# Kernel tuning notes

Measured on AMD Instinct MI355X. Metric: run time of the kernel, lower is better.

## Reference

```python
import jax, jax.numpy as jnp
import numpy as np

EPS = 1e-6
N_HEADS = 16


def _stable_softmax(x):
    # max subtracted with stop_gradient (torch .detach()), clamp to [-50, 50], eps in denom
    x_max = jax.lax.stop_gradient(jnp.max(x, axis=-1, keepdims=True))
    exp_x = jnp.exp(jnp.clip(x - x_max, -50.0, 50.0))
    return exp_x / (jnp.sum(exp_x, axis=-1, keepdims=True) + EPS)


def setup_inputs() -> dict:
    key = jax.random.key(0)
    k1, k2, k3 = jax.random.split(key, 3)
    B, S, D = 2, 2048, 1024
    x = jax.random.normal(k1, (B, S, D), dtype=jnp.float32)
    Wqkv = jax.random.normal(k2, (3 * D, D), dtype=jnp.float32) * 0.02
    Wout = jax.random.normal(k3, (D, D), dtype=jnp.float32) * (0.02 / np.sqrt(2))
    return {"x": x, "Wqkv": Wqkv, "Wout": Wout}


def reference(x, Wqkv, Wout):
    B, S, D = x.shape
    H = N_HEADS
    Dh = D // H
    scale = 1.0 / np.sqrt(Dh)
    # qkv projection (torch Linear: x @ W.T), split into q,k,v -> (B,H,S,Dh)
    qkv = (x @ Wqkv.T).reshape(B, S, 3, H, Dh)
    qkv = jnp.transpose(qkv, (2, 0, 3, 1, 4))
    q, k, v = qkv[0], qkv[1], qkv[2]
    # chunked attention is mathematically identical to full attention here
    scores = jnp.einsum('bhqd,bhkd->bhqk', q, k) * scale
    attn = _stable_softmax(scores)
    out = jnp.einsum('bhqk,bhkd->bhqd', attn, v)  # (B,H,S,Dh)
    out = jnp.transpose(out, (0, 2, 1, 3)).reshape(B, S, D)
    return out @ Wout.T
```

## Files before the change

kernel.cpp:

```cpp
#include <hip/hip_runtime.h>
#include <hip/hip_bf16.h>
#include <stdint.h>

#define S_LEN   2048
#define D_MODEL 1024
#define NH      16
#define DH      64
#define BATCH   2
#define TOKENS  (BATCH * S_LEN)

typedef __bf16 bf16;
typedef __bf16 bf16x8 __attribute__((ext_vector_type(8)));
typedef __bf16 b16x4  __attribute__((ext_vector_type(4)));
typedef float  f32x4  __attribute__((ext_vector_type(4)));
typedef float  f32x16 __attribute__((ext_vector_type(16)));
typedef unsigned int uint32;

__device__ __forceinline__ void async_lds16(const void* g, void* l) {
  __builtin_amdgcn_global_load_lds((__attribute__((address_space(1))) void*)g,
                                   (__attribute__((address_space(3))) void*)l,
                                   16, 0, 0);
}

__global__ __launch_bounds__(256) void convert_kernel(
    const float* __restrict__ src, bf16* __restrict__ dst, int n8) {
  const int i = blockIdx.x * 256 + threadIdx.x;
  if (i >= n8) return;
  const f32x4 a = *(const f32x4*)(src + (size_t)i * 8);
  const f32x4 b = *(const f32x4*)(src + (size_t)i * 8 + 4);
  bf16x8 o;
#pragma unroll
  for (int j = 0; j < 4; j++) { o[j] = (bf16)a[j]; o[j + 4] = (bf16)b[j]; }
  *(bf16x8*)(dst + (size_t)i * 8) = o;
}

#define BM 128
#define BN 128
#define BK 32

#define GEMM_CORE(APTR, BPTR, KDIM)                                              \
  __shared__ __align__(16) bf16 As[BM * BK];                                     \
  __shared__ __align__(16) bf16 Bs[BN * BK];                                     \
  const int tid  = threadIdx.x;                                                  \
  const int wave = tid >> 6, lane = tid & 63;                                    \
  const int quad = lane >> 4, l16 = lane & 15;                                   \
  const int m0 = blockIdx.y * BM;                                                \
  const int n0 = blockIdx.x * BN;                                                \
  const int wm = (wave >> 1) * 64, wn = (wave & 1) * 64;                         \
  f32x4 acc[4][4] = {};                                                          \
  const int c0 = tid, c1 = tid + 256;                                            \
  for (int k0 = 0; k0 < (KDIM); k0 += BK) {                                      \
    async_lds16((APTR) + (size_t)(m0 + (c0 >> 2)) * (KDIM) + k0 + (c0 & 3) * 8,  \
                As + c0 * 8);                                                    \
    async_lds16((APTR) + (size_t)(m0 + (c1 >> 2)) * (KDIM) + k0 + (c1 & 3) * 8,  \
                As + c1 * 8);                                                    \
    async_lds16((BPTR) + (size_t)(n0 + (c0 >> 2)) * (KDIM) + k0 + (c0 & 3) * 8,  \
                Bs + c0 * 8);                                                    \
    async_lds16((BPTR) + (size_t)(n0 + (c1 >> 2)) * (KDIM) + k0 + (c1 & 3) * 8,  \
                Bs + c1 * 8);                                                    \
    __syncthreads();                                                             \
    bf16x8 af[4], bfr[4];                                                        \
    _Pragma("unroll") for (int i = 0; i < 4; i++)                                \
        af[i] = *(const bf16x8*)(As + (wm + i * 16 + l16) * BK + quad * 8);      \
    _Pragma("unroll") for (int j = 0; j < 4; j++)                                \
        bfr[j] = *(const bf16x8*)(Bs + (wn + j * 16 + l16) * BK + quad * 8);     \
    _Pragma("unroll") for (int i = 0; i < 4; i++)                                \
      _Pragma("unroll") for (int j = 0; j < 4; j++)                              \
        acc[i][j] = __builtin_amdgcn_mfma_f32_16x16x32_bf16(af[i], bfr[j],       \
                                                            acc[i][j], 0, 0, 0); \
    __syncthreads();                                                             \
  }

__global__ __launch_bounds__(256) void gemm_qkv_kernel(
    const bf16* __restrict__ X, const bf16* __restrict__ W,
    bf16* __restrict__ Qo, bf16* __restrict__ Ko, bf16* __restrict__ VTo) {
  GEMM_CORE(X, W, D_MODEL)
  const int t = n0 >> 10;
#pragma unroll
  for (int i = 0; i < 4; i++) {
    const int rowb = m0 + wm + i * 16 + quad * 4;
    const int b = rowb >> 11, s0 = rowb & 2047;
#pragma unroll
    for (int j = 0; j < 4; j++) {
      const int col = n0 + wn + j * 16 + l16;
      const int h = (col >> 6) & 15, d = col & 63;
      if (t == 2) {
        b16x4 v4;
#pragma unroll
        for (int r = 0; r < 4; r++) v4[r] = (bf16)acc[i][j][r];
        *(b16x4*)(VTo + ((size_t)(b * NH + h) * DH + d) * S_LEN + s0) = v4;
      } else {
#pragma unroll
        for (int r = 0; r < 4; r++) {
          const float v = acc[i][j][r];
          if (t == 0)
            Qo[((size_t)(b * NH + h) * S_LEN + s0 + r) * DH + d] = (bf16)(v * 0.125f);
          else
            Ko[((size_t)(b * NH + h) * S_LEN + s0 + r) * DH + d] = (bf16)v;
        }
      }
    }
  }
}

__global__ __launch_bounds__(256) void gemm_out_kernel(
    const bf16* __restrict__ A, const bf16* __restrict__ W,
    float* __restrict__ Out) {
  GEMM_CORE(A, W, D_MODEL)
#pragma unroll
  for (int i = 0; i < 4; i++) {
    const int rowb = m0 + wm + i * 16 + quad * 4;
#pragma unroll
    for (int j = 0; j < 4; j++) {
      const int col = n0 + wn + j * 16 + l16;
#pragma unroll
      for (int r = 0; r < 4; r++)
        Out[(size_t)(rowb + r) * D_MODEL + col] = acc[i][j][r];
    }
  }
}

__global__ __launch_bounds__(512, 4) void attn_kernel(
    const bf16* __restrict__ Q, const bf16* __restrict__ K,
    const bf16* __restrict__ VT, bf16* __restrict__ AO) {
  __shared__ __align__(16) bf16 smem[2][2][2 * 64 * 64];

  const int tid  = threadIdx.x;
  const int lane = tid & 63;
  const int wave = tid >> 6;
  const int g    = wave >> 2;
  const int qw   = wave & 3;
  const int l31  = lane & 31;
  const int hi   = lane >> 5;
  const int sw   = l31 & 7;

  const int bid = (blockIdx.x & 7) * 64 + (blockIdx.x >> 3);
  const int qb  = bid & 15;
  const int bh  = bid >> 4;

  const bf16* qp = Q  + ((size_t)bh * S_LEN + qb * 128 + qw * 32 + l31) * DH;
  const bf16* kp = K  + (size_t)bh * S_LEN * DH;
  const bf16* vp = VT + (size_t)bh * DH * S_LEN;

  bf16x8 qf[4];
#pragma unroll
  for (int dk = 0; dk < 4; dk++)
    qf[dk] = *(const bf16x8*)(qp + dk * 16 + hi * 8);

  const int gtid = tid & 255;
  const int cid0 = gtid, cid1 = gtid + 256;
  const int r0 = cid0 >> 3, c0 = (cid0 & 7) ^ (r0 & 7);
  const int r1 = cid1 >> 3, c1 = (cid1 & 7) ^ (r1 & 7);
  const bf16* ka0 = kp + (size_t)(g * 64 + r0) * DH + c0 * 8;
  const bf16* ka1 = kp + (size_t)(g * 64 + r1) * DH + c1 * 8;
  const bf16* va0 = vp + (size_t)r0 * S_LEN + g * 64 + c0 * 8;
  const bf16* va1 = vp + (size_t)r1 * S_LEN + g * 64 + c1 * 8;
  const int ld0 = cid0 * 8, ld1 = cid1 * 8;

  f32x16 oT[2] = {};
  float lsum = 0.f;

  bf16* sg = &smem[g][0][0];

#define STAGE(B)                                                                 \
  {                                                                              \
    bf16* s = sg + (B) * (2 * 64 * 64);                                          \
    async_lds16(ka0, s + ld0);                                                   \
    async_lds16(ka1, s + ld1);                                                   \
    async_lds16(va0, s + 4096 + ld0);                                            \
    async_lds16(va1, s + 4096 + ld1);                                            \
    ka0 += 8192; ka1 += 8192; va0 += 128; va1 += 128;                            \
  }

  STAGE(0)

  for (int t = 0; t < 16; t++) {
    const int cur = t & 1;
    if (t < 15) {
      STAGE(cur ^ 1)
      asm volatile("s_waitcnt vmcnt(4)" ::: "memory");
    } else {
      asm volatile("s_waitcnt vmcnt(0)" ::: "memory");
    }
    __builtin_amdgcn_s_barrier();
    __builtin_amdgcn_s_setprio(1);

    const bf16* sb = sg + cur * (2 * 64 * 64);

    f32x16 st[2] = {};
#pragma unroll
    for (int kt = 0; kt < 2; kt++)
#pragma unroll
      for (int dk = 0; dk < 4; dk++) {
        const bf16x8 kf = *(const bf16x8*)(sb + (kt * 32 + l31) * 64 +
                                           (((dk * 2 + hi) ^ sw) * 8));
        st[kt] = __builtin_amdgcn_mfma_f32_32x32x16_bf16(kf, qf[dk], st[kt], 0, 0, 0);
      }

#pragma unroll
    for (int kt = 0; kt < 2; kt++)
#pragma unroll
      for (int half = 0; half < 2; half++) {
        float e[8];
#pragma unroll
        for (int r = 0; r < 8; r++) e[r] = __expf(st[kt][half * 8 + r]);
        lsum += ((e[0] + e[1]) + (e[2] + e[3])) + ((e[4] + e[5]) + (e[6] + e[7]));
        uint32 a0, a1, b0, b1;
        asm("v_cvt_pk_bf16_f32 %0, %1, %2" : "=v"(a0) : "v"(e[0]), "v"(e[1]));
        asm("v_cvt_pk_bf16_f32 %0, %1, %2" : "=v"(a1) : "v"(e[2]), "v"(e[3]));
        asm("v_cvt_pk_bf16_f32 %0, %1, %2" : "=v"(b0) : "v"(e[4]), "v"(e[5]));
        asm("v_cvt_pk_bf16_f32 %0, %1, %2" : "=v"(b1) : "v"(e[6]), "v"(e[7]));
        asm("v_permlane32_swap_b32 %0, %1" : "+v"(a0), "+v"(b0));
        asm("v_permlane32_swap_b32 %0, %1" : "+v"(a1), "+v"(b1));
        union { uint32 u[4]; bf16x8 v; } pf;
        pf.u[0] = a0; pf.u[1] = a1; pf.u[2] = b0; pf.u[3] = b1;
        const int ks = kt * 2 + half;
#pragma unroll
        for (int dt = 0; dt < 2; dt++) {
          const bf16x8 vf = *(const bf16x8*)(sb + 4096 + (dt * 32 + l31) * 64 +
                                             (((ks * 2 + hi) ^ sw) * 8));
          oT[dt] = __builtin_amdgcn_mfma_f32_32x32x16_bf16(vf, pf.v, oT[dt], 0, 0, 0);
        }
      }

    __builtin_amdgcn_s_setprio(0);
    asm volatile("s_waitcnt lgkmcnt(0)" ::: "memory");
    __builtin_amdgcn_s_barrier();
  }
#undef STAGE

  lsum += __shfl_xor(lsum, 32);

  float* mO = (float*)&smem[0][0][0];
  float* mL = mO + 4 * 64 * 32;
  const int mrow = qw * 64 + lane;
  if (g == 1) {
#pragma unroll
    for (int j = 0; j < 8; j++) {
      const int dt = j >> 2, rb = (j & 3) * 4;
      f32x4 c = { oT[dt][rb], oT[dt][rb + 1], oT[dt][rb + 2], oT[dt][rb + 3] };
      *(f32x4*)((char*)mO + mrow * 128 + ((j ^ (lane & 7)) * 16)) = c;
    }
    mL[mrow] = lsum;
  }
  __syncthreads();
  if (g == 0) {
#pragma unroll
    for (int j = 0; j < 8; j++) {
      const int dt = j >> 2, rb = (j & 3) * 4;
      const f32x4 c = *(const f32x4*)((char*)mO + mrow * 128 + ((j ^ (lane & 7)) * 16));
#pragma unroll
      for (int rr = 0; rr < 4; rr++) oT[dt][rb + rr] += c[rr];
    }
    lsum += mL[mrow];
    const float inv = 1.0f / (lsum + 1e-6f);
    const int b = bh >> 4, h = bh & 15;
    const int srow = qb * 128 + qw * 32 + l31;
    const size_t base = (size_t)(b * S_LEN + srow) * D_MODEL + h * DH;
#pragma unroll
    for (int dt = 0; dt < 2; dt++)
#pragma unroll
      for (int rg = 0; rg < 4; rg++) {
        b16x4 o4;
#pragma unroll
        for (int rr = 0; rr < 4; rr++) o4[rr] = (bf16)(oT[dt][rg * 4 + rr] * inv);
        *(b16x4*)(AO + base + dt * 32 + rg * 8 + hi * 4) = o4;
      }
  }
}

extern "C" void kernel_launch(void* const* d_in, const int* in_sizes, int n_in,
                              void* d_out, int out_size, void* d_ws, size_t ws_size,
                              hipStream_t stream) {
  const float* x    = (const float*)d_in[0];
  const float* wqkv = (const float*)d_in[1];
  const float* wout = (const float*)d_in[2];
  float* out = (float*)d_out;

  bf16* Q  = (bf16*)d_ws;
  bf16* K  = Q  + (size_t)TOKENS * D_MODEL;
  bf16* VT = K  + (size_t)TOKENS * D_MODEL;
  bf16* xb = VT + (size_t)TOKENS * D_MODEL;
  bf16* AO = xb;
  bf16* wqkvb = (bf16*)d_out;
  bf16* woutb = Q;

  convert_kernel<<<dim3(TOKENS * D_MODEL / (256 * 8)), dim3(256), 0, stream>>>(
      x, xb, TOKENS * D_MODEL / 8);
  convert_kernel<<<dim3(3 * D_MODEL * D_MODEL / (256 * 8)), dim3(256), 0, stream>>>(
      wqkv, wqkvb, 3 * D_MODEL * D_MODEL / 8);

  gemm_qkv_kernel<<<dim3(3 * D_MODEL / BN, TOKENS / BM), dim3(256), 0, stream>>>(
      xb, wqkvb, Q, K, VT);

  attn_kernel<<<dim3(BATCH * NH * (S_LEN / 128)), dim3(512), 0, stream>>>(Q, K, VT, AO);

  convert_kernel<<<dim3(D_MODEL * D_MODEL / (256 * 8)), dim3(256), 0, stream>>>(
      wout, woutb, D_MODEL * D_MODEL / 8);

  gemm_out_kernel<<<dim3(D_MODEL / BN, TOKENS / BM), dim3(256), 0, stream>>>(
      AO, woutb, out);
}
```

Baseline: 187.9 us.

## Process two 32-row query tiles per wave in attention to reuse K/V fragments

Each attention wave now handles 64 query rows (two 32-row MFMA tiles) instead of 32, so each block covers 256 queries and the grid is halved. Every K and V fragment read from LDS feeds two MFMAs, which halves LDS traffic and global K/V staging per query. The cost is double the accumulator registers, so launch bounds drop to 2 blocks per CU, and the cross-group merge now takes two serialized rounds through shared memory. Fewer blocks (256) may underfill the GPU's compute units.

```diff
diff --git a/kernel.cpp b/kernel.cpp
--- a/kernel.cpp
+++ b/kernel.cpp
@@ -120,7 +120,7 @@
   }
 }
 
-__global__ __launch_bounds__(512, 4) void attn_kernel(
+__global__ __launch_bounds__(512, 2) void attn_kernel(
     const bf16* __restrict__ Q, const bf16* __restrict__ K,
     const bf16* __restrict__ VT, bf16* __restrict__ AO) {
   __shared__ __align__(16) bf16 smem[2][2][2 * 64 * 64];
@@ -134,18 +134,20 @@
   const int hi   = lane >> 5;
   const int sw   = l31 & 7;
 
-  const int bid = (blockIdx.x & 7) * 64 + (blockIdx.x >> 3);
-  const int qb  = bid & 15;
-  const int bh  = bid >> 4;
-
-  const bf16* qp = Q  + ((size_t)bh * S_LEN + qb * 128 + qw * 32 + l31) * DH;
+  const int bid = (blockIdx.x & 7) * 32 + (blockIdx.x >> 3);
+  const int qb  = bid & 7;
+  const int bh  = bid >> 3;
+
+  const bf16* qp = Q  + ((size_t)bh * S_LEN + qb * 256 + qw * 64 + l31) * DH;
   const bf16* kp = K  + (size_t)bh * S_LEN * DH;
   const bf16* vp = VT + (size_t)bh * DH * S_LEN;
 
-  bf16x8 qf[4];
-#pragma unroll
-  for (int dk = 0; dk < 4; dk++)
-    qf[dk] = *(const bf16x8*)(qp + dk * 16 + hi * 8);
+  bf16x8 qf0[4], qf1[4];
+#pragma unroll
+  for (int dk = 0; dk < 4; dk++) {
+    qf0[dk] = *(const bf16x8*)(qp + dk * 16 + hi * 8);
+    qf1[dk] = *(const bf16x8*)(qp + 32 * DH + dk * 16 + hi * 8);
+  }
 
   const int gtid = tid & 255;
   const int cid0 = gtid, cid1 = gtid + 256;
@@ -157,8 +159,8 @@
   const bf16* va1 = vp + (size_t)r1 * S_LEN + g * 64 + c1 * 8;
   const int ld0 = cid0 * 8, ld1 = cid1 * 8;
 
-  f32x16 oT[2] = {};
-  float lsum = 0.f;
+  f32x16 oT0[2] = {}, oT1[2] = {};
+  float lsum0 = 0.f, lsum1 = 0.f;
 
   bf16* sg = &smem[g][0][0];
 
@@ -187,39 +189,51 @@
 
     const bf16* sb = sg + cur * (2 * 64 * 64);
 
-    f32x16 st[2] = {};
+    f32x16 st0[2] = {}, st1[2] = {};
 #pragma unroll
     for (int kt = 0; kt < 2; kt++)
 #pragma unroll
       for (int dk = 0; dk < 4; dk++) {
         const bf16x8 kf = *(const bf16x8*)(sb + (kt * 32 + l31) * 64 +
                                            (((dk * 2 + hi) ^ sw) * 8));
-        st[kt] = __builtin_amdgcn_mfma_f32_32x32x16_bf16(kf, qf[dk], st[kt], 0, 0, 0);
+        st0[kt] = __builtin_amdgcn_mfma_f32_32x32x16_bf16(kf, qf0[dk], st0[kt], 0, 0, 0);
+        st1[kt] = __builtin_amdgcn_mfma_f32_32x32x16_bf16(kf, qf1[dk], st1[kt], 0, 0, 0);
       }
 
 #pragma unroll
     for (int kt = 0; kt < 2; kt++)
 #pragma unroll
-      for (int half = 0; half < 2; half++) {
-        float e[8];
-#pragma unroll
-        for (int r = 0; r < 8; r++) e[r] = __expf(st[kt][half * 8 + r]);
-        lsum += ((e[0] + e[1]) + (e[2] + e[3])) + ((e[4] + e[5]) + (e[6] + e[7]));
-        uint32 a0, a1, b0, b1;
-        asm("v_cvt_pk_bf16_f32 %0, %1, %2" : "=v"(a0) : "v"(e[0]), "v"(e[1]));
-        asm("v_cvt_pk_bf16_f32 %0, %1, %2" : "=v"(a1) : "v"(e[2]), "v"(e[3]));
-        asm("v_cvt_pk_bf16_f32 %0, %1, %2" : "=v"(b0) : "v"(e[4]), "v"(e[5]));
-        asm("v_cvt_pk_bf16_f32 %0, %1, %2" : "=v"(b1) : "v"(e[6]), "v"(e[7]));
-        asm("v_permlane32_swap_b32 %0, %1" : "+v"(a0), "+v"(b0));
-        asm("v_permlane32_swap_b32 %0, %1" : "+v"(a1), "+v"(b1));
-        union { uint32 u[4]; bf16x8 v; } pf;
-        pf.u[0] = a0; pf.u[1] = a1; pf.u[2] = b0; pf.u[3] = b1;
-        const int ks = kt * 2 + half;
+      for (int hk = 0; hk < 2; hk++) {
+        const int ks = kt * 2 + hk;
+        float e0[8], e1[8];
+#pragma unroll
+        for (int r = 0; r < 8; r++) e0[r] = __expf(st0[kt][hk * 8 + r]);
+#pragma unroll
+        for (int r = 0; r < 8; r++) e1[r] = __expf(st1[kt][hk * 8 + r]);
+        lsum0 += ((e0[0] + e0[1]) + (e0[2] + e0[3])) + ((e0[4] + e0[5]) + (e0[6] + e0[7]));
+        lsum1 += ((e1[0] + e1[1]) + (e1[2] + e1[3])) + ((e1[4] + e1[5]) + (e1[6] + e1[7]));
+        uint32 p00, p01, p02, p03, p10, p11, p12, p13;
+        asm("v_cvt_pk_bf16_f32 %0, %1, %2" : "=v"(p00) : "v"(e0[0]), "v"(e0[1]));
+        asm("v_cvt_pk_bf16_f32 %0, %1, %2" : "=v"(p01) : "v"(e0[2]), "v"(e0[3]));
+        asm("v_cvt_pk_bf16_f32 %0, %1, %2" : "=v"(p02) : "v"(e0[4]), "v"(e0[5]));
+        asm("v_cvt_pk_bf16_f32 %0, %1, %2" : "=v"(p03) : "v"(e0[6]), "v"(e0[7]));
+        asm("v_cvt_pk_bf16_f32 %0, %1, %2" : "=v"(p10) : "v"(e1[0]), "v"(e1[1]));
+        asm("v_cvt_pk_bf16_f32 %0, %1, %2" : "=v"(p11) : "v"(e1[2]), "v"(e1[3]));
+        asm("v_cvt_pk_bf16_f32 %0, %1, %2" : "=v"(p12) : "v"(e1[4]), "v"(e1[5]));
+        asm("v_cvt_pk_bf16_f32 %0, %1, %2" : "=v"(p13) : "v"(e1[6]), "v"(e1[7]));
+        asm("v_permlane32_swap_b32 %0, %1" : "+v"(p00), "+v"(p02));
+        asm("v_permlane32_swap_b32 %0, %1" : "+v"(p01), "+v"(p03));
+        asm("v_permlane32_swap_b32 %0, %1" : "+v"(p10), "+v"(p12));
+        asm("v_permlane32_swap_b32 %0, %1" : "+v"(p11), "+v"(p13));
+        union { uint32 u[4]; bf16x8 v; } pf0, pf1;
+        pf0.u[0] = p00; pf0.u[1] = p01; pf0.u[2] = p02; pf0.u[3] = p03;
+        pf1.u[0] = p10; pf1.u[1] = p11; pf1.u[2] = p12; pf1.u[3] = p13;
 #pragma unroll
         for (int dt = 0; dt < 2; dt++) {
           const bf16x8 vf = *(const bf16x8*)(sb + 4096 + (dt * 32 + l31) * 64 +
                                              (((ks * 2 + hi) ^ sw) * 8));
-          oT[dt] = __builtin_amdgcn_mfma_f32_32x32x16_bf16(vf, pf.v, oT[dt], 0, 0, 0);
+          oT0[dt] = __builtin_amdgcn_mfma_f32_32x32x16_bf16(vf, pf0.v, oT0[dt], 0, 0, 0);
+          oT1[dt] = __builtin_amdgcn_mfma_f32_32x32x16_bf16(vf, pf1.v, oT1[dt], 0, 0, 0);
         }
       }
 
@@ -229,19 +243,21 @@
   }
 #undef STAGE
 
-  lsum += __shfl_xor(lsum, 32);
+  lsum0 += __shfl_xor(lsum0, 32);
+  lsum1 += __shfl_xor(lsum1, 32);
 
   float* mO = (float*)&smem[0][0][0];
-  float* mL = mO + 4 * 64 * 32;
+  float* mL = mO + 256 * 32;
   const int mrow = qw * 64 + lane;
+
   if (g == 1) {
 #pragma unroll
     for (int j = 0; j < 8; j++) {
       const int dt = j >> 2, rb = (j & 3) * 4;
-      f32x4 c = { oT[dt][rb], oT[dt][rb + 1], oT[dt][rb + 2], oT[dt][rb + 3] };
+      f32x4 c = { oT0[dt][rb], oT0[dt][rb + 1], oT0[dt][rb + 2], oT0[dt][rb + 3] };
       *(f32x4*)((char*)mO + mrow * 128 + ((j ^ (lane & 7)) * 16)) = c;
     }
-    mL[mrow] = lsum;
+    mL[mrow] = lsum0;
   }
   __syncthreads();
   if (g == 0) {
@@ -250,21 +266,54 @@
       const int dt = j >> 2, rb = (j & 3) * 4;
       const f32x4 c = *(const f32x4*)((char*)mO + mrow * 128 + ((j ^ (lane & 7)) * 16));
 #pragma unroll
-      for (int rr = 0; rr < 4; rr++) oT[dt][rb + rr] += c[rr];
-    }
-    lsum += mL[mrow];
-    const float inv = 1.0f / (lsum + 1e-6f);
+      for (int rr = 0; rr < 4; rr++) oT0[dt][rb + rr] += c[rr];
+    }
+    lsum0 += mL[mrow];
+  }
+  __syncthreads();
+  if (g == 1) {
+#pragma unroll
+    for (int j = 0; j < 8; j++) {
+      const int dt = j >> 2, rb = (j & 3) * 4;
+      f32x4 c = { oT1[dt][rb], oT1[dt][rb + 1], oT1[dt][rb + 2], oT1[dt][rb + 3] };
+      *(f32x4*)((char*)mO + mrow * 128 + ((j ^ (lane & 7)) * 16)) = c;
+    }
+    mL[mrow] = lsum1;
+  }
+  __syncthreads();
+  if (g == 0) {
+#pragma unroll
+    for (int j = 0; j < 8; j++) {
+      const int dt = j >> 2, rb = (j & 3) * 4;
+      const f32x4 c = *(const f32x4*)((char*)mO + mrow * 128 + ((j ^ (lane & 7)) * 16));
+#pragma unroll
+      for (int rr = 0; rr < 4; rr++) oT1[dt][rb + rr] += c[rr];
+    }
+    lsum1 += mL[mrow];
+
+    const float inv0 = 1.0f / (lsum0 + 1e-6f);
+    const float inv1 = 1.0f / (lsum1 + 1e-6f);
     const int b = bh >> 4, h = bh & 15;
-    const int srow = qb * 128 + qw * 32 + l31;
-    const size_t base = (size_t)(b * S_LEN + srow) * D_MODEL + h * DH;
+    const int srow = qb * 256 + qw * 64 + l31;
+    const size_t base0 = (size_t)(b * S_LEN + srow) * D_MODEL + h * DH;
+    const size_t base1 = base0 + (size_t)32 * D_MODEL;
 #pragma unroll
     for (int dt = 0; dt < 2; dt++)
 #pragma unroll
       for (int rg = 0; rg < 4; rg++) {
         b16x4 o4;
 #pragma unroll
-        for (int rr = 0; rr < 4; rr++) o4[rr] = (bf16)(oT[dt][rg * 4 + rr] * inv);
-        *(b16x4*)(AO + base + dt * 32 + rg * 8 + hi * 4) = o4;
+        for (int rr = 0; rr < 4; rr++) o4[rr] = (bf16)(oT0[dt][rg * 4 + rr] * inv0);
+        *(b16x4*)(AO + base0 + dt * 32 + rg * 8 + hi * 4) = o4;
+      }
+#pragma unroll
+    for (int dt = 0; dt < 2; dt++)
+#pragma unroll
+      for (int rg = 0; rg < 4; rg++) {
+        b16x4 o4;
+#pragma unroll
+        for (int rr = 0; rr < 4; rr++) o4[rr] = (bf16)(oT1[dt][rg * 4 + rr] * inv1);
+        *(b16x4*)(AO + base1 + dt * 32 + rg * 8 + hi * 4) = o4;
       }
   }
 }
@@ -293,7 +342,7 @@
   gemm_qkv_kernel<<<dim3(3 * D_MODEL / BN, TOKENS / BM), dim3(256), 0, stream>>>(
       xb, wqkvb, Q, K, VT);
 
-  attn_kernel<<<dim3(BATCH * NH * (S_LEN / 128)), dim3(512), 0, stream>>>(Q, K, VT, AO);
+  attn_kernel<<<dim3(BATCH * NH * (S_LEN / 256)), dim3(512), 0, stream>>>(Q, K, VT, AO);
 
   convert_kernel<<<dim3(D_MODEL * D_MODEL / (256 * 8)), dim3(256), 0, stream>>>(
       wout, woutb, D_MODEL * D_MODEL / 8);
```

Result: no change. 186.6 us (-0.7%).
